# Kernel optimization log

Measured on AMD Instinct MI355X. Metric: run time of the kernel, lower is better.

## Reference

```python
import jax, jax.numpy as jnp
import numpy as np

B, L, D = 2, 512, 128

def setup_inputs() -> dict:
    key = jax.random.key(0)
    ks = jax.random.split(key, 5)
    scale = 1.0 / np.sqrt(D)
    return {
        "s": jax.random.normal(ks[0], (B, L, D), dtype=jnp.float32),
        "h": jax.random.normal(ks[1], (B, L, D), dtype=jnp.float32),
        "W": jax.random.normal(ks[2], (D, D), dtype=jnp.float32) * scale,
        "U": jax.random.normal(ks[3], (D, D), dtype=jnp.float32) * scale,
        "v": jax.random.normal(ks[4], (D, 1), dtype=jnp.float32) * scale,
    }

def reference(s, h, W, U, v):
    # s, h: [B, L, D]; W, U: [D, D]; v: [D, 1]
    sW = s @ W                      # [B, L, D]
    hU = h @ U                      # [B, L, D]
    # additive scores: tanh(sW_i + hU_j) . v  -> [B, L, L]
    scores = jnp.einsum("blmd,d->blm", jnp.tanh(sW[:, :, None, :] + hU[:, None, :, :]), v[:, 0])
    attn = jax.nn.softmax(scores, axis=-1)   # softmax over keys (last axis)
    # dropout p=0 is identity; weighted sum over h
    return jnp.einsum("blm,bmd->bld", attn, h)
```

## Files before the change

kernel.cpp:

```cpp
#include <hip/hip_runtime.h>

#define DD 128
#define LL 512
#define BB 2
#define NK (BB * LL)

__global__ __launch_bounds__(256)
void proj_kernel(const float* __restrict__ s, const float* __restrict__ h,
                 const float* __restrict__ W, const float* __restrict__ U,
                 float* __restrict__ swB, float* __restrict__ huT4) {
    __shared__ float xr[4 * DD];
    int bx = blockIdx.x;
    bool second = bx >= 256;
    const float* X = second ? h : s;
    const float* M = second ? U : W;
    int row0 = (bx & 255) * 4;
    int t = threadIdx.x;
    xr[t]       = X[row0 * DD + t];
    xr[t + 256] = X[row0 * DD + 256 + t];
    __syncthreads();
    int c = t & 127, g = t >> 7;
    const float* x0 = &xr[(2 * g) * DD];
    const float* x1 = &xr[(2 * g + 1) * DD];
    float a0 = 0.f, a1 = 0.f;
#pragma unroll 8
    for (int d = 0; d < DD; ++d) {
        float m = M[d * DD + c];
        a0 = fmaf(x0[d], m, a0);
        a1 = fmaf(x1[d], m, a1);
    }
    a0 *= 2.0f; a1 *= 2.0f;
    if (!second) {
        swB[(row0 + 2 * g) * DD + c]     = a0;
        swB[(row0 + 2 * g + 1) * DD + c] = a1;
    } else {
        int base = (c >> 2) * (NK * 4) + (c & 3);
        huT4[base + (row0 + 2 * g) * 4]     = a0;
        huT4[base + (row0 + 2 * g + 1) * 4] = a1;
    }
}

__global__ __launch_bounds__(512, 4)
void attn_kernel(const float* __restrict__ swB, const float* __restrict__ huT4,
                 const float* __restrict__ h, const float* __restrict__ v,
                 float* __restrict__ out) {
    __shared__ float2 p2[LL];
    __shared__ float2 wsum[8];
    __shared__ float red[8][2][DD];

    int bx = blockIdx.x;
    int row0 = bx * 2;
    int b = bx >> 8;
    int t = threadIdx.x;
    int lane = t & 63;
    int w = __builtin_amdgcn_readfirstlane(t >> 6);

    int j = w * 64 + lane;
    int kk = b * LL + j;
    const float4* hp = (const float4*)huT4 + kk;
    const float* sw0 = swB + (size_t)row0 * DD;
    const float* sw1 = sw0 + DD;
    float acc0 = 0.f, acc1 = 0.f;
#pragma unroll 4
    for (int dg = 0; dg < 32; ++dg) {
        float4 hv = hp[(size_t)dg * NK];
        float4 s0 = *(const float4*)(sw0 + dg * 4);
        float4 s1 = *(const float4*)(sw1 + dg * 4);
        float4 vv = *(const float4*)(v   + dg * 4);
        acc0 = fmaf(vv.x, __builtin_amdgcn_rcpf(__expf(s0.x + hv.x) + 1.f), acc0);
        acc0 = fmaf(vv.y, __builtin_amdgcn_rcpf(__expf(s0.y + hv.y) + 1.f), acc0);
        acc0 = fmaf(vv.z, __builtin_amdgcn_rcpf(__expf(s0.z + hv.z) + 1.f), acc0);
        acc0 = fmaf(vv.w, __builtin_amdgcn_rcpf(__expf(s0.w + hv.w) + 1.f), acc0);
        acc1 = fmaf(vv.x, __builtin_amdgcn_rcpf(__expf(s1.x + hv.x) + 1.f), acc1);
        acc1 = fmaf(vv.y, __builtin_amdgcn_rcpf(__expf(s1.y + hv.y) + 1.f), acc1);
        acc1 = fmaf(vv.z, __builtin_amdgcn_rcpf(__expf(s1.z + hv.z) + 1.f), acc1);
        acc1 = fmaf(vv.w, __builtin_amdgcn_rcpf(__expf(s1.w + hv.w) + 1.f), acc1);
    }
    float p0 = __expf(-2.f * acc0);
    float p1 = __expf(-2.f * acc1);
    p2[j] = make_float2(p0, p1);
    float sm0 = p0, sm1 = p1;
#pragma unroll
    for (int o = 1; o < 64; o <<= 1) {
        sm0 += __shfl_xor(sm0, o);
        sm1 += __shfl_xor(sm1, o);
    }
    if (lane == 0) wsum[w] = make_float2(sm0, sm1);
    __syncthreads();

    int half = lane >> 5;
    int d4 = (lane & 31) * 4;
    const float* hb = h + (size_t)b * LL * DD;
    float4 a0 = make_float4(0.f, 0.f, 0.f, 0.f);
    float4 a1 = make_float4(0.f, 0.f, 0.f, 0.f);
#pragma unroll 4
    for (int jj = 0; jj < 32; ++jj) {
        int jl = w * 64 + jj * 2 + half;
        float4 hv = *(const float4*)&hb[jl * DD + d4];
        float2 pp = p2[jl];
        a0.x = fmaf(pp.x, hv.x, a0.x);  a1.x = fmaf(pp.y, hv.x, a1.x);
        a0.y = fmaf(pp.x, hv.y, a0.y);  a1.y = fmaf(pp.y, hv.y, a1.y);
        a0.z = fmaf(pp.x, hv.z, a0.z);  a1.z = fmaf(pp.y, hv.z, a1.z);
        a0.w = fmaf(pp.x, hv.w, a0.w);  a1.w = fmaf(pp.y, hv.w, a1.w);
    }
    a0.x += __shfl_xor(a0.x, 32);  a0.y += __shfl_xor(a0.y, 32);
    a0.z += __shfl_xor(a0.z, 32);  a0.w += __shfl_xor(a0.w, 32);
    a1.x += __shfl_xor(a1.x, 32);  a1.y += __shfl_xor(a1.y, 32);
    a1.z += __shfl_xor(a1.z, 32);  a1.w += __shfl_xor(a1.w, 32);
    if (half == 0) {
        *(float4*)&red[w][0][d4] = a0;
        *(float4*)&red[w][1][d4] = a1;
    }
    __syncthreads();

    if (t < 256) {
        int q = t >> 7, d = t & 127;
        float o = 0.f;
#pragma unroll
        for (int k = 0; k < 8; ++k) o += red[k][q][d];
        float qs = 0.f;
#pragma unroll
        for (int k = 0; k < 8; ++k) qs += (q == 0) ? wsum[k].x : wsum[k].y;
        out[(size_t)(row0 + q) * DD + d] = o * __builtin_amdgcn_rcpf(qs);
    }
}

extern "C" void kernel_launch(void* const* d_in, const int* in_sizes, int n_in,
                              void* d_out, int out_size, void* d_ws, size_t ws_size,
                              hipStream_t stream) {
    const float* s = (const float*)d_in[0];
    const float* h = (const float*)d_in[1];
    const float* W = (const float*)d_in[2];
    const float* U = (const float*)d_in[3];
    const float* v = (const float*)d_in[4];
    float* out = (float*)d_out;
    float* ws  = (float*)d_ws;

    float* swB  = ws;
    float* huT4 = ws + 131072;

    hipLaunchKernelGGL(proj_kernel, dim3(512), dim3(256), 0, stream,
                       s, h, W, U, swB, huT4);
    hipLaunchKernelGGL(attn_kernel, dim3(NK / 2), dim3(512), 0, stream,
                       swB, huT4, h, v, out);
}
```

Before: 86.10 us.

## Precompute exponentials of projections and pair tanh terms to share one reciprocal

The projection kernel now stores exp(2·sW) and exp(2·hU), so the score loop multiplies two exponentials instead of calling exp once per element. Pairs of tanh terms are combined over a common denominator, so one reciprocal serves two dimensions. Each attention block now handles four query rows instead of two, which halves the grid and reuses each hU load across more rows. In exchange, exp of unbounded projections can overflow or lose precision for large inputs, and the larger accumulator set lowers the occupancy hint from 4 to 2.

```diff
diff --git a/kernel.cpp b/kernel.cpp
--- a/kernel.cpp
+++ b/kernel.cpp
@@ -8,7 +8,7 @@
 __global__ __launch_bounds__(256)
 void proj_kernel(const float* __restrict__ s, const float* __restrict__ h,
                  const float* __restrict__ W, const float* __restrict__ U,
-                 float* __restrict__ swB, float* __restrict__ huT4) {
+                 float* __restrict__ Es, float* __restrict__ EhT4) {
     __shared__ float xr[4 * DD];
     int bx = blockIdx.x;
     bool second = bx >= 256;
@@ -16,8 +16,8 @@
     const float* M = second ? U : W;
     int row0 = (bx & 255) * 4;
     int t = threadIdx.x;
-    xr[t]       = X[row0 * DD + t];
-    xr[t + 256] = X[row0 * DD + 256 + t];
+    xr[t]       = 2.0f * X[row0 * DD + t];
+    xr[t + 256] = 2.0f * X[row0 * DD + 256 + t];
     __syncthreads();
     int c = t & 127, g = t >> 7;
     const float* x0 = &xr[(2 * g) * DD];
@@ -29,98 +29,125 @@
         a0 = fmaf(x0[d], m, a0);
         a1 = fmaf(x1[d], m, a1);
     }
-    a0 *= 2.0f; a1 *= 2.0f;
+    float e0 = __expf(a0);
+    float e1 = __expf(a1);
     if (!second) {
-        swB[(row0 + 2 * g) * DD + c]     = a0;
-        swB[(row0 + 2 * g + 1) * DD + c] = a1;
+        Es[(row0 + 2 * g) * DD + c]     = e0;
+        Es[(row0 + 2 * g + 1) * DD + c] = e1;
     } else {
         int base = (c >> 2) * (NK * 4) + (c & 3);
-        huT4[base + (row0 + 2 * g) * 4]     = a0;
-        huT4[base + (row0 + 2 * g + 1) * 4] = a1;
+        EhT4[base + (row0 + 2 * g) * 4]     = e0;
+        EhT4[base + (row0 + 2 * g + 1) * 4] = e1;
     }
 }
 
-__global__ __launch_bounds__(512, 4)
-void attn_kernel(const float* __restrict__ swB, const float* __restrict__ huT4,
+__global__ __launch_bounds__(512, 2)
+void attn_kernel(const float* __restrict__ Es, const float* __restrict__ EhT4,
                  const float* __restrict__ h, const float* __restrict__ v,
                  float* __restrict__ out) {
-    __shared__ float2 p2[LL];
-    __shared__ float2 wsum[8];
-    __shared__ float red[8][2][DD];
+    __shared__ float4 p4[LL];
+    __shared__ float4 wsum4[8];
+    __shared__ float red[8][4][DD];
 
     int bx = blockIdx.x;
-    int row0 = bx * 2;
-    int b = bx >> 8;
+    int row0 = bx * 4;
+    int b = bx >> 7;
     int t = threadIdx.x;
     int lane = t & 63;
     int w = __builtin_amdgcn_readfirstlane(t >> 6);
 
     int j = w * 64 + lane;
     int kk = b * LL + j;
-    const float4* hp = (const float4*)huT4 + kk;
-    const float* sw0 = swB + (size_t)row0 * DD;
-    const float* sw1 = sw0 + DD;
-    float acc0 = 0.f, acc1 = 0.f;
+    const float4* hp = (const float4*)EhT4 + kk;
+    const float* es0 = Es + (size_t)row0 * DD;
+    float ac0 = 0.f, ac1 = 0.f, ac2 = 0.f, ac3 = 0.f;
+    float cc0 = 0.f, cc1 = 0.f, cc2 = 0.f, cc3 = 0.f;
 #pragma unroll 4
     for (int dg = 0; dg < 32; ++dg) {
-        float4 hv = hp[(size_t)dg * NK];
-        float4 s0 = *(const float4*)(sw0 + dg * 4);
-        float4 s1 = *(const float4*)(sw1 + dg * 4);
-        float4 vv = *(const float4*)(v   + dg * 4);
-        acc0 = fmaf(vv.x, __builtin_amdgcn_rcpf(__expf(s0.x + hv.x) + 1.f), acc0);
-        acc0 = fmaf(vv.y, __builtin_amdgcn_rcpf(__expf(s0.y + hv.y) + 1.f), acc0);
-        acc0 = fmaf(vv.z, __builtin_amdgcn_rcpf(__expf(s0.z + hv.z) + 1.f), acc0);
-        acc0 = fmaf(vv.w, __builtin_amdgcn_rcpf(__expf(s0.w + hv.w) + 1.f), acc0);
-        acc1 = fmaf(vv.x, __builtin_amdgcn_rcpf(__expf(s1.x + hv.x) + 1.f), acc1);
-        acc1 = fmaf(vv.y, __builtin_amdgcn_rcpf(__expf(s1.y + hv.y) + 1.f), acc1);
-        acc1 = fmaf(vv.z, __builtin_amdgcn_rcpf(__expf(s1.z + hv.z) + 1.f), acc1);
-        acc1 = fmaf(vv.w, __builtin_amdgcn_rcpf(__expf(s1.w + hv.w) + 1.f), acc1);
+        float4 E  = hp[(size_t)dg * NK];
+        float4 q0 = *(const float4*)(es0 + 0 * DD + dg * 4);
+        float4 q1 = *(const float4*)(es0 + 1 * DD + dg * 4);
+        float4 q2 = *(const float4*)(es0 + 2 * DD + dg * 4);
+        float4 q3 = *(const float4*)(es0 + 3 * DD + dg * 4);
+        float4 vv = *(const float4*)(v + dg * 4);
+        float vsxy = vv.x + vv.y;
+        float vszw = vv.z + vv.w;
+#define PAIR(eqx, eqy, Ehx, Ehy, vx, vy, vs, ACC, CCC)                    \
+        {                                                                 \
+            float Ex = eqx * Ehx;                                         \
+            float Ey = eqy * Ehy;                                         \
+            float uy = Ey + 1.f;                                          \
+            float den = fmaf(Ex, uy, uy);                                 \
+            float r = __builtin_amdgcn_rcpf(den);                         \
+            float num = fmaf(vx, Ey, vy * Ex);                            \
+            ACC = fmaf(num, r, ACC);                                      \
+            CCC = fmaf(vs, r, CCC);                                       \
+        }
+        PAIR(q0.x, q0.y, E.x, E.y, vv.x, vv.y, vsxy, ac0, cc0)
+        PAIR(q0.z, q0.w, E.z, E.w, vv.z, vv.w, vszw, ac0, cc0)
+        PAIR(q1.x, q1.y, E.x, E.y, vv.x, vv.y, vsxy, ac1, cc1)
+        PAIR(q1.z, q1.w, E.z, E.w, vv.z, vv.w, vszw, ac1, cc1)
+        PAIR(q2.x, q2.y, E.x, E.y, vv.x, vv.y, vsxy, ac2, cc2)
+        PAIR(q2.z, q2.w, E.z, E.w, vv.z, vv.w, vszw, ac2, cc2)
+        PAIR(q3.x, q3.y, E.x, E.y, vv.x, vv.y, vsxy, ac3, cc3)
+        PAIR(q3.z, q3.w, E.z, E.w, vv.z, vv.w, vszw, ac3, cc3)
+#undef PAIR
     }
-    float p0 = __expf(-2.f * acc0);
-    float p1 = __expf(-2.f * acc1);
-    p2[j] = make_float2(p0, p1);
-    float sm0 = p0, sm1 = p1;
+    float p0 = __expf(-2.f * (ac0 + cc0));
+    float p1 = __expf(-2.f * (ac1 + cc1));
+    float p2 = __expf(-2.f * (ac2 + cc2));
+    float p3 = __expf(-2.f * (ac3 + cc3));
+    p4[j] = make_float4(p0, p1, p2, p3);
+    float m0 = p0, m1 = p1, m2 = p2, m3 = p3;
 #pragma unroll
     for (int o = 1; o < 64; o <<= 1) {
-        sm0 += __shfl_xor(sm0, o);
-        sm1 += __shfl_xor(sm1, o);
+        m0 += __shfl_xor(m0, o);
+        m1 += __shfl_xor(m1, o);
+        m2 += __shfl_xor(m2, o);
+        m3 += __shfl_xor(m3, o);
     }
-    if (lane == 0) wsum[w] = make_float2(sm0, sm1);
+    if (lane == 0) wsum4[w] = make_float4(m0, m1, m2, m3);
     __syncthreads();
 
     int half = lane >> 5;
     int d4 = (lane & 31) * 4;
     const float* hb = h + (size_t)b * LL * DD;
-    float4 a0 = make_float4(0.f, 0.f, 0.f, 0.f);
-    float4 a1 = make_float4(0.f, 0.f, 0.f, 0.f);
+    float4 A0 = make_float4(0.f, 0.f, 0.f, 0.f), A1 = A0, A2 = A0, A3 = A0;
 #pragma unroll 4
     for (int jj = 0; jj < 32; ++jj) {
         int jl = w * 64 + jj * 2 + half;
         float4 hv = *(const float4*)&hb[jl * DD + d4];
-        float2 pp = p2[jl];
-        a0.x = fmaf(pp.x, hv.x, a0.x);  a1.x = fmaf(pp.y, hv.x, a1.x);
-        a0.y = fmaf(pp.x, hv.y, a0.y);  a1.y = fmaf(pp.y, hv.y, a1.y);
-        a0.z = fmaf(pp.x, hv.z, a0.z);  a1.z = fmaf(pp.y, hv.z, a1.z);
-        a0.w = fmaf(pp.x, hv.w, a0.w);  a1.w = fmaf(pp.y, hv.w, a1.w);
+        float4 pp = p4[jl];
+        A0.x = fmaf(pp.x, hv.x, A0.x); A0.y = fmaf(pp.x, hv.y, A0.y);
+        A0.z = fmaf(pp.x, hv.z, A0.z); A0.w = fmaf(pp.x, hv.w, A0.w);
+        A1.x = fmaf(pp.y, hv.x, A1.x); A1.y = fmaf(pp.y, hv.y, A1.y);
+        A1.z = fmaf(pp.y, hv.z, A1.z); A1.w = fmaf(pp.y, hv.w, A1.w);
+        A2.x = fmaf(pp.z, hv.x, A2.x); A2.y = fmaf(pp.z, hv.y, A2.y);
+        A2.z = fmaf(pp.z, hv.z, A2.z); A2.w = fmaf(pp.z, hv.w, A2.w);
+        A3.x = fmaf(pp.w, hv.x, A3.x); A3.y = fmaf(pp.w, hv.y, A3.y);
+        A3.z = fmaf(pp.w, hv.z, A3.z); A3.w = fmaf(pp.w, hv.w, A3.w);
     }
-    a0.x += __shfl_xor(a0.x, 32);  a0.y += __shfl_xor(a0.y, 32);
-    a0.z += __shfl_xor(a0.z, 32);  a0.w += __shfl_xor(a0.w, 32);
-    a1.x += __shfl_xor(a1.x, 32);  a1.y += __shfl_xor(a1.y, 32);
-    a1.z += __shfl_xor(a1.z, 32);  a1.w += __shfl_xor(a1.w, 32);
+#define FOLD(A) A.x += __shfl_xor(A.x, 32); A.y += __shfl_xor(A.y, 32); \
+                A.z += __shfl_xor(A.z, 32); A.w += __shfl_xor(A.w, 32);
+    FOLD(A0) FOLD(A1) FOLD(A2) FOLD(A3)
+#undef FOLD
     if (half == 0) {
-        *(float4*)&red[w][0][d4] = a0;
-        *(float4*)&red[w][1][d4] = a1;
+        *(float4*)&red[w][0][d4] = A0;
+        *(float4*)&red[w][1][d4] = A1;
+        *(float4*)&red[w][2][d4] = A2;
+        *(float4*)&red[w][3][d4] = A3;
     }
     __syncthreads();
 
-    if (t < 256) {
+    {
         int q = t >> 7, d = t & 127;
         float o = 0.f;
 #pragma unroll
         for (int k = 0; k < 8; ++k) o += red[k][q][d];
+        const float* wf = (const float*)wsum4;
         float qs = 0.f;
 #pragma unroll
-        for (int k = 0; k < 8; ++k) qs += (q == 0) ? wsum[k].x : wsum[k].y;
+        for (int k = 0; k < 8; ++k) qs += wf[k * 4 + q];
         out[(size_t)(row0 + q) * DD + d] = o * __builtin_amdgcn_rcpf(qs);
     }
 }
@@ -136,11 +163,11 @@
     float* out = (float*)d_out;
     float* ws  = (float*)d_ws;
 
-    float* swB  = ws;
-    float* huT4 = ws + 131072;
+    float* Es   = ws;
+    float* EhT4 = ws + 131072;
 
     hipLaunchKernelGGL(proj_kernel, dim3(512), dim3(256), 0, stream,
-                       s, h, W, U, swB, huT4);
-    hipLaunchKernelGGL(attn_kernel, dim3(NK / 2), dim3(512), 0, stream,
-                       swB, huT4, h, v, out);
+                       s, h, W, U, Es, EhT4);
+    hipLaunchKernelGGL(attn_kernel, dim3(NK / 4), dim3(512), 0, stream,
+                       Es, EhT4, h, v, out);
 }
```

Result: faster. 81.61 us, median of 2 (-5.2%).
